# Performance work log

Measured on AMD Instinct MI355X. Metric: run time of the kernel, lower is better.

The kernel has to match this reference:

```python
import jax, jax.numpy as jnp
import numpy as np

N_SRC, N_DST, E = 100000, 50000, 1000000
IN_F, H, D = 256, 4, 32
NEG_SLOPE = 0.2


def setup_inputs() -> dict:
    key = jax.random.key(0)
    k = jax.random.split(key, 7)
    x = jax.random.normal(k[0], (N_SRC, IN_F), dtype=jnp.float32)
    # scale weights so exp() of attention logits stays well-conditioned
    fc_w = jax.random.normal(k[1], (H * D, IN_F), dtype=jnp.float32) * (1.0 / np.sqrt(IN_F))
    attn_l = jax.random.normal(k[2], (1, H, D), dtype=jnp.float32) * 0.1
    attn_r = jax.random.normal(k[3], (1, H, D), dtype=jnp.float32) * 0.1
    src_idx = jax.random.randint(k[4], (E,), 0, N_SRC, dtype=jnp.int32)
    dst_idx = jax.random.randint(k[5], (E,), 0, N_DST, dtype=jnp.int32)
    dst_node_ids = jax.random.randint(k[6], (N_DST,), 0, N_SRC, dtype=jnp.int32)
    return {"x": x, "fc_w": fc_w, "attn_l": attn_l, "attn_r": attn_r,
            "src_idx": src_idx, "dst_idx": dst_idx, "dst_node_ids": dst_node_ids}


def reference(x, fc_w, attn_l, attn_r, src_idx, dst_idx, dst_node_ids):
    # fc: [N_src, in] @ [in, H*D] -> [N_src, H, D]
    h = (x @ fc_w.T).reshape(-1, H, D)
    # per-node, per-head attention scalars
    el = jnp.einsum('nhd,ohd->nh', h, attn_l)            # [N_src, H]
    h_dst = h[dst_node_ids]                               # self_gather -> [N_dst, H, D]
    er = jnp.einsum('nhd,ohd->nh', h_dst, attn_r)        # [N_dst, H]
    # apply_edge: e = el[src] + er[dst], then leaky_relu + exp (edge softmax numerator)
    e = el[src_idx] + er[dst_idx]                         # [E, H]
    e = jnp.where(e >= 0, e, NEG_SLOPE * e)
    exp_e = jnp.exp(e)
    # apply_node: segment-sum denominators over destination nodes
    sum_exp = jax.ops.segment_sum(exp_e, dst_idx, num_segments=N_DST)  # [N_dst, H]
    att = exp_e / sum_exp[dst_idx]                        # [E, H]
    # attention_gather: weighted scatter-add of source features to dst nodes
    msg = att[:, :, None] * h[src_idx]                    # [E, H, D]
    out = jax.ops.segment_sum(msg, dst_idx, num_segments=N_DST)        # [N_dst, H, D]
    return out.reshape(N_DST, H * D)
```

## Files before the change

kernel.cpp:

```cpp
#include <hip/hip_runtime.h>
#include <hip/hip_bf16.h>

#define N_SRC_N  100000
#define N_DST_N  50000
#define NE       1000000
#define IN_F     256
#define NH       4
#define ND       32
#define HD       128
#define NEG_SLOPE 0.2f
#define L2E      1.44269504f

#define DPB      32
#define NB       1563
#define CAP      1024

typedef __attribute__((ext_vector_type(8))) short short8v;
typedef __attribute__((ext_vector_type(4))) short short4v;
typedef __attribute__((ext_vector_type(4))) float f32x4;

__device__ __forceinline__ short f2bf(float f) {
    __hip_bfloat16 h = __float2bfloat16(f);
    return *reinterpret_cast<short*>(&h);
}
__device__ __forceinline__ float bflo(unsigned u) { return __uint_as_float(u << 16); }
__device__ __forceinline__ float bfhi(unsigned u) { return __uint_as_float(u & 0xffff0000u); }

__global__ __launch_bounds__(256) void cvt_w(const float* __restrict__ w,
                                             short* __restrict__ wb)
{
    int i4 = blockIdx.x * 256 + threadIdx.x;
    if (i4 < (HD * IN_F) / 4) {
        f32x4 v = ((const f32x4*)w)[i4];
        short4v s;
        s[0] = f2bf(v[0]); s[1] = f2bf(v[1]); s[2] = f2bf(v[2]); s[3] = f2bf(v[3]);
        ((short4v*)wb)[i4] = s;
    }
}

__global__ __launch_bounds__(256) void gemm_fc_mfma(
    const float* __restrict__ x, const short* __restrict__ wb,
    const float* __restrict__ al, short* __restrict__ hb,
    float* __restrict__ el)
{
    __shared__ short wlds[HD * IN_F];

    const int tid = threadIdx.x;
    {
        int row = tid >> 1, half = tid & 1;
#pragma unroll
        for (int c = 0; c < 16; ++c) {
            int chunk = half * 16 + c;
            short8v v = *(const short8v*)(wb + row * IN_F + chunk * 8);
            int boff = (chunk * 16) ^ ((row & 7) << 4);
            *(short8v*)((char*)wlds + row * 512 + boff) = v;
        }
    }
    __syncthreads();

    const int w  = tid >> 6;
    const int l  = tid & 63;
    const int lr = l & 15;
    const int lk = l >> 4;

    float alv[8];
#pragma unroll
    for (int ct = 0; ct < 8; ++ct) alv[ct] = al[ct * 16 + lr];

    const int wave_id = blockIdx.x * 4 + w;
    for (int tile = wave_id; tile < N_SRC_N / 16; tile += 2048) {
        const int row0 = tile * 16;
        const float* xp = x + (size_t)(row0 + lr) * IN_F + lk * 8;

        f32x4 a[16];
#pragma unroll
        for (int kk = 0; kk < 8; ++kk) {
            a[2 * kk]     = *(const f32x4*)(xp + kk * 32);
            a[2 * kk + 1] = *(const f32x4*)(xp + kk * 32 + 4);
        }
        __builtin_amdgcn_sched_barrier(0);

        f32x4 acc[8];
#pragma unroll
        for (int ct = 0; ct < 8; ++ct) acc[ct] = (f32x4){0.f, 0.f, 0.f, 0.f};

#pragma unroll
        for (int kk = 0; kk < 8; ++kk) {
            f32x4 u0 = a[2 * kk], u1 = a[2 * kk + 1];
            short8v af;
            af[0] = f2bf(u0[0]); af[1] = f2bf(u0[1]);
            af[2] = f2bf(u0[2]); af[3] = f2bf(u0[3]);
            af[4] = f2bf(u1[0]); af[5] = f2bf(u1[1]);
            af[6] = f2bf(u1[2]); af[7] = f2bf(u1[3]);
            const int boff = (kk * 64 + lk * 16) ^ ((lr & 7) << 4);
#pragma unroll
            for (int ct = 0; ct < 8; ++ct) {
                short8v bf = *(const short8v*)((const char*)wlds
                                               + (ct * 16 + lr) * 512 + boff);
                acc[ct] = __builtin_amdgcn_mfma_f32_16x16x32_bf16(af, bf, acc[ct], 0, 0, 0);
            }
        }

#pragma unroll
        for (int r = 0; r < 4; ++r) {
            short* hp = hb + (size_t)(row0 + lk * 4 + r) * HD + lr;
#pragma unroll
            for (int ct = 0; ct < 8; ++ct) hp[ct * 16] = f2bf(acc[ct][r]);
        }

#pragma unroll
        for (int h = 0; h < 4; ++h) {
            float p[4];
#pragma unroll
            for (int r = 0; r < 4; ++r)
                p[r] = acc[2 * h][r] * alv[2 * h] + acc[2 * h + 1][r] * alv[2 * h + 1];
#pragma unroll
            for (int o = 1; o < 16; o <<= 1) {
#pragma unroll
                for (int r = 0; r < 4; ++r) p[r] += __shfl_xor(p[r], o, 64);
            }
            if (lr == 0) {
#pragma unroll
                for (int r = 0; r < 4; ++r)
                    el[(row0 + lk * 4 + r) * NH + h] = p[r];
            }
        }
    }
}

__global__ __launch_bounds__(256) void er_kernel(
    const short* __restrict__ hb, const float* __restrict__ ar,
    const int* __restrict__ dnid, float* __restrict__ er, int ndst)
{
    int i = blockIdx.x * 4 + (threadIdx.x >> 6);
    if (i >= ndst) return;
    int l = threadIdx.x & 63;
    int n = dnid[i];
    unsigned u = *(const unsigned*)(hb + (size_t)n * HD + 2 * l);
    float s = bflo(u) * ar[2 * l] + bfhi(u) * ar[2 * l + 1];
#pragma unroll
    for (int o = 1; o < 16; o <<= 1) s += __shfl_xor(s, o, 64);
    if ((l & 15) == 0) er[i * NH + (l >> 4)] = s;
}

__global__ __launch_bounds__(256) void bucket_hist(
    const int4* __restrict__ dst4, int* __restrict__ bcnt, int n4)
{
    __shared__ int lh[NB];
    for (int i = threadIdx.x; i < NB; i += 256) lh[i] = 0;
    __syncthreads();
#pragma unroll
    for (int q = 0; q < 4; ++q) {
        int e4 = blockIdx.x * 1024 + q * 256 + threadIdx.x;
        if (e4 < n4) {
            int4 v = dst4[e4];
            atomicAdd(&lh[v.x >> 5], 1); atomicAdd(&lh[v.y >> 5], 1);
            atomicAdd(&lh[v.z >> 5], 1); atomicAdd(&lh[v.w >> 5], 1);
        }
    }
    __syncthreads();
    for (int i = threadIdx.x; i < NB; i += 256) {
        int c = lh[i];
        if (c > 0) atomicAdd(&bcnt[i], c);
    }
}

__global__ __launch_bounds__(1024) void bucket_scan(
    const int* __restrict__ bcnt, int* __restrict__ boff, int* __restrict__ bcur, int n)
{
    int tid = threadIdx.x;
    int i0 = 2 * tid, i1 = 2 * tid + 1;
    int a = (i0 < n) ? bcnt[i0] : 0;
    int c = (i1 < n) ? bcnt[i1] : 0;
    int s = a + c, v = s;
#pragma unroll
    for (int o = 1; o < 64; o <<= 1) {
        int t = __shfl_up(v, o, 64);
        if ((tid & 63) >= o) v += t;
    }
    __shared__ int ws[16];
    if ((tid & 63) == 63) ws[tid >> 6] = v;
    __syncthreads();
    int add = 0;
    for (int q = 0; q < (tid >> 6); ++q) add += ws[q];
    int excl = v - s + add;
    if (i0 < n) { boff[i0] = excl;     bcur[i0] = excl; }
    if (i1 < n) { boff[i1] = excl + a; bcur[i1] = excl + a; }
}

__global__ __launch_bounds__(256) void partition(
    const int4* __restrict__ src4, const int4* __restrict__ dst4,
    int* __restrict__ bcur, int* __restrict__ ebuf, int n4)
{
    __shared__ int lh[NB];
    __shared__ int base[NB];
    for (int i = threadIdx.x; i < NB; i += 256) lh[i] = 0;
    __syncthreads();
    int4 sv[4], dv[4];
#pragma unroll
    for (int q = 0; q < 4; ++q) {
        int e4 = blockIdx.x * 1024 + q * 256 + threadIdx.x;
        if (e4 < n4) {
            sv[q] = src4[e4]; dv[q] = dst4[e4];
            atomicAdd(&lh[dv[q].x >> 5], 1); atomicAdd(&lh[dv[q].y >> 5], 1);
            atomicAdd(&lh[dv[q].z >> 5], 1); atomicAdd(&lh[dv[q].w >> 5], 1);
        } else {
            dv[q].x = -1;
        }
    }
    __syncthreads();
    for (int i = threadIdx.x; i < NB; i += 256) {
        int cnt = lh[i];
        base[i] = (cnt > 0) ? atomicAdd(&bcur[i], cnt) : 0;
        lh[i] = 0;
    }
    __syncthreads();
#pragma unroll
    for (int q = 0; q < 4; ++q) {
        if (dv[q].x < 0) continue;
        int ss[4] = {sv[q].x, sv[q].y, sv[q].z, sv[q].w};
        int dd[4] = {dv[q].x, dv[q].y, dv[q].z, dv[q].w};
#pragma unroll
        for (int j = 0; j < 4; ++j) {
            int b = dd[j] >> 5;
            int off = atomicAdd(&lh[b], 1);
            ebuf[base[b] + off] = ss[j] | ((dd[j] & 31) << 17);
        }
    }
}

__global__ __launch_bounds__(256) void gat_gather(
    const short* __restrict__ hb, const float* __restrict__ el,
    const float* __restrict__ er, const int* __restrict__ ebuf,
    const int* __restrict__ bcnt, const int* __restrict__ boff,
    float* __restrict__ out, int ndst)
{
    __shared__ int stage_[CAP];
    __shared__ int ssrc[CAP];
    __shared__ int lh[DPB];
    __shared__ int loff[DPB + 1];
    __shared__ int curs[DPB];

    const int b = blockIdx.x;
    const int tid = threadIdx.x;
    const int cnt = bcnt[b];
    const int gbase = boff[b];
    const int lcnt = (cnt < CAP) ? cnt : CAP;

    if (tid < DPB) lh[tid] = 0;
    __syncthreads();
    for (int i = tid; i < lcnt; i += 256) {
        int p = ebuf[gbase + i];
        stage_[i] = p;
        atomicAdd(&lh[(p >> 17) & 31], 1);
    }
    __syncthreads();
    if (tid < DPB) {
        int v = lh[tid];
#pragma unroll
        for (int o = 1; o < 32; o <<= 1) {
            int t = __shfl_up(v, o, 64);
            if (tid >= o) v += t;
        }
        loff[tid + 1] = v;
        if (tid == 0) loff[0] = 0;
    }
    __syncthreads();
    if (tid < DPB) curs[tid] = loff[tid];
    __syncthreads();
    for (int i = tid; i < lcnt; i += 256) {
        int p = stage_[i];
        int dl = (p >> 17) & 31;
        int pos = atomicAdd(&curs[dl], 1);
        ssrc[pos] = (p & 0x1FFFF) << 8;
    }
    __syncthreads();

    const int wv = tid >> 6;
    const int l  = tid & 63;
    const int head = l >> 4;
    const char* hbase = (const char*)hb + 4 * l;
    const char* ebase = (const char*)el + head * 4;

    for (int dl = wv; dl < DPB; dl += 4) {
        int d = b * DPB + dl;
        if (d >= ndst) continue;
        int j0 = loff[dl], j1 = loff[dl + 1];
        float erv = er[d * NH + head];

        float sumA = 0.f, sumB = 0.f;
        float acc0A = 0.f, acc1A = 0.f, acc0B = 0.f, acc1B = 0.f;
        int j = j0;
        for (; j + 8 <= j1; j += 8) {
            int off[8]; unsigned u[8]; float ev[8];
#pragma unroll
            for (int q = 0; q < 8; ++q) off[q] = ssrc[j + q];
#pragma unroll
            for (int q = 0; q < 8; ++q)
                u[q] = *(const unsigned*)(hbase + off[q]);
#pragma unroll
            for (int q = 0; q < 8; ++q)
                ev[q] = *(const float*)(ebase + (off[q] >> 4));
#pragma unroll
            for (int q = 0; q < 8; ++q) {
                float e = ev[q] + erv;
                e = fmaxf(e, NEG_SLOPE * e);
                float wq = __expf(e);
                if (q & 1) {
                    sumB += wq;
                    acc0B = fmaf(wq, bflo(u[q]), acc0B);
                    acc1B = fmaf(wq, bfhi(u[q]), acc1B);
                } else {
                    sumA += wq;
                    acc0A = fmaf(wq, bflo(u[q]), acc0A);
                    acc1A = fmaf(wq, bfhi(u[q]), acc1A);
                }
            }
        }
        for (; j < j1; ++j) {
            int off0 = ssrc[j];
            unsigned u0 = *(const unsigned*)(hbase + off0);
            float e0 = *(const float*)(ebase + (off0 >> 4)) + erv;
            e0 = fmaxf(e0, NEG_SLOPE * e0);
            float w0 = __expf(e0);
            sumA += w0;
            acc0A = fmaf(w0, bflo(u0), acc0A); acc1A = fmaf(w0, bfhi(u0), acc1A);
        }
        if (cnt > CAP) {
            for (int t = CAP; t < cnt; ++t) {
                int p = ebuf[gbase + t];
                if (((p >> 17) & 31) == dl) {
                    int off0 = (p & 0x1FFFF) << 8;
                    unsigned u0 = *(const unsigned*)(hbase + off0);
                    float e0 = *(const float*)(ebase + (off0 >> 4)) + erv;
                    e0 = fmaxf(e0, NEG_SLOPE * e0);
                    float w0 = __expf(e0);
                    sumA += w0;
                    acc0A = fmaf(w0, bflo(u0), acc0A); acc1A = fmaf(w0, bfhi(u0), acc1A);
                }
            }
        }
        float sum = sumA + sumB;
        bool any = (j1 > j0) || (cnt > CAP);
        float inv = any ? 1.f / sum : 0.f;
        float2 o2 = make_float2((acc0A + acc0B) * inv, (acc1A + acc1B) * inv);
        *(float2*)(out + (size_t)d * HD + 2 * l) = o2;
    }
}

extern "C" void kernel_launch(void* const* d_in, const int* in_sizes, int n_in,
                              void* d_out, int out_size, void* d_ws, size_t ws_size,
                              hipStream_t stream)
{
    const float* x   = (const float*)d_in[0];
    const float* fw  = (const float*)d_in[1];
    const float* al  = (const float*)d_in[2];
    const float* ar  = (const float*)d_in[3];
    const int*   src = (const int*)d_in[4];
    const int*   dst = (const int*)d_in[5];
    const int*   dnid= (const int*)d_in[6];
    float* out = (float*)d_out;

    char* ws = (char*)d_ws;
    size_t off = 0;
    auto alloc = [&](size_t bytes) -> void* {
        void* p = ws + off;
        off = (off + bytes + 255) & ~(size_t)255;
        return p;
    };
    short* hb   = (short*)alloc((size_t)N_SRC_N * HD * sizeof(short));
    short* wb   = (short*)alloc((size_t)HD * IN_F * sizeof(short));
    float* el   = (float*)alloc((size_t)N_SRC_N * NH * sizeof(float));
    float* er   = (float*)alloc((size_t)N_DST_N * NH * sizeof(float));
    int*   ebuf = (int*)alloc((size_t)NE * sizeof(int));
    int*   bcnt = (int*)alloc((size_t)NB * sizeof(int));
    int*   boff = (int*)alloc((size_t)NB * sizeof(int));
    int*   bcur = (int*)alloc((size_t)NB * sizeof(int));

    hipMemsetAsync(bcnt, 0, (size_t)NB * sizeof(int), stream);

    cvt_w<<<(HD * IN_F / 4 + 255) / 256, 256, 0, stream>>>(fw, wb);
    gemm_fc_mfma<<<512, 256, 0, stream>>>(x, wb, al, hb, el);
    er_kernel<<<(N_DST_N + 3) / 4, 256, 0, stream>>>(hb, ar, dnid, er, N_DST_N);
    bucket_hist<<<(NE / 4 + 1023) / 1024, 256, 0, stream>>>((const int4*)dst, bcnt, NE / 4);
    bucket_scan<<<1, 1024, 0, stream>>>(bcnt, boff, bcur, NB);
    partition<<<(NE / 4 + 1023) / 1024, 256, 0, stream>>>((const int4*)src, (const int4*)dst,
                                                          bcur, ebuf, NE / 4);
    gat_gather<<<NB, 256, 0, stream>>>(hb, el, er, ebuf, bcnt, boff, out, N_DST_N);
}
```

Baseline: 130.4 us.

## Fuse er computation into gather, widen GEMM blocks and partition chunks

Drops the separate er_kernel and computes each destination's er score inside gat_gather by loading the gathered node's bf16 features and reducing against attn_r with wave shuffles. This removes one launch and the er buffer round trip. The GEMM now runs 512-thread blocks with 8 waves sharing each LDS weight copy. The partition kernel handles twice as many edges per block, halving its grid and the number of global bucket-cursor atomics. The trade-offs are register pressure in partition (8 int4 pairs held per thread) and fewer waves in flight for that kernel.

```diff
diff --git a/kernel.cpp b/kernel.cpp
--- a/kernel.cpp
+++ b/kernel.cpp
@@ -9,7 +9,6 @@
 #define ND       32
 #define HD       128
 #define NEG_SLOPE 0.2f
-#define L2E      1.44269504f
 
 #define DPB      32
 #define NB       1563
@@ -38,7 +37,7 @@
     }
 }
 
-__global__ __launch_bounds__(256) void gemm_fc_mfma(
+__global__ __launch_bounds__(512, 4) void gemm_fc_mfma(
     const float* __restrict__ x, const short* __restrict__ wb,
     const float* __restrict__ al, short* __restrict__ hb,
     float* __restrict__ el)
@@ -47,10 +46,10 @@
 
     const int tid = threadIdx.x;
     {
-        int row = tid >> 1, half = tid & 1;
-#pragma unroll
-        for (int c = 0; c < 16; ++c) {
-            int chunk = half * 16 + c;
+        int row = tid >> 2, qt = tid & 3;
+#pragma unroll
+        for (int c = 0; c < 8; ++c) {
+            int chunk = qt * 8 + c;
             short8v v = *(const short8v*)(wb + row * IN_F + chunk * 8);
             int boff = (chunk * 16) ^ ((row & 7) << 4);
             *(short8v*)((char*)wlds + row * 512 + boff) = v;
@@ -67,8 +66,8 @@
 #pragma unroll
     for (int ct = 0; ct < 8; ++ct) alv[ct] = al[ct * 16 + lr];
 
-    const int wave_id = blockIdx.x * 4 + w;
-    for (int tile = wave_id; tile < N_SRC_N / 16; tile += 2048) {
+    const int wave_id = blockIdx.x * 8 + w;
+    for (int tile = wave_id; tile < N_SRC_N / 16; tile += 4096) {
         const int row0 = tile * 16;
         const float* xp = x + (size_t)(row0 + lr) * IN_F + lk * 8;
 
@@ -128,21 +127,6 @@
     }
 }
 
-__global__ __launch_bounds__(256) void er_kernel(
-    const short* __restrict__ hb, const float* __restrict__ ar,
-    const int* __restrict__ dnid, float* __restrict__ er, int ndst)
-{
-    int i = blockIdx.x * 4 + (threadIdx.x >> 6);
-    if (i >= ndst) return;
-    int l = threadIdx.x & 63;
-    int n = dnid[i];
-    unsigned u = *(const unsigned*)(hb + (size_t)n * HD + 2 * l);
-    float s = bflo(u) * ar[2 * l] + bfhi(u) * ar[2 * l + 1];
-#pragma unroll
-    for (int o = 1; o < 16; o <<= 1) s += __shfl_xor(s, o, 64);
-    if ((l & 15) == 0) er[i * NH + (l >> 4)] = s;
-}
-
 __global__ __launch_bounds__(256) void bucket_hist(
     const int4* __restrict__ dst4, int* __restrict__ bcnt, int n4)
 {
@@ -196,10 +180,10 @@
     __shared__ int base[NB];
     for (int i = threadIdx.x; i < NB; i += 256) lh[i] = 0;
     __syncthreads();
-    int4 sv[4], dv[4];
-#pragma unroll
-    for (int q = 0; q < 4; ++q) {
-        int e4 = blockIdx.x * 1024 + q * 256 + threadIdx.x;
+    int4 sv[8], dv[8];
+#pragma unroll
+    for (int q = 0; q < 8; ++q) {
+        int e4 = blockIdx.x * 2048 + q * 256 + threadIdx.x;
         if (e4 < n4) {
             sv[q] = src4[e4]; dv[q] = dst4[e4];
             atomicAdd(&lh[dv[q].x >> 5], 1); atomicAdd(&lh[dv[q].y >> 5], 1);
@@ -216,7 +200,7 @@
     }
     __syncthreads();
 #pragma unroll
-    for (int q = 0; q < 4; ++q) {
+    for (int q = 0; q < 8; ++q) {
         if (dv[q].x < 0) continue;
         int ss[4] = {sv[q].x, sv[q].y, sv[q].z, sv[q].w};
         int dd[4] = {dv[q].x, dv[q].y, dv[q].z, dv[q].w};
@@ -231,9 +215,9 @@
 
 __global__ __launch_bounds__(256) void gat_gather(
     const short* __restrict__ hb, const float* __restrict__ el,
-    const float* __restrict__ er, const int* __restrict__ ebuf,
-    const int* __restrict__ bcnt, const int* __restrict__ boff,
-    float* __restrict__ out, int ndst)
+    const float* __restrict__ ar, const int* __restrict__ dnid,
+    const int* __restrict__ ebuf, const int* __restrict__ bcnt,
+    const int* __restrict__ boff, float* __restrict__ out, int ndst)
 {
     __shared__ int stage_[CAP];
     __shared__ int ssrc[CAP];
@@ -281,12 +265,18 @@
     const int head = l >> 4;
     const char* hbase = (const char*)hb + 4 * l;
     const char* ebase = (const char*)el + head * 4;
+    const float ar0 = ar[2 * l], ar1 = ar[2 * l + 1];
 
     for (int dl = wv; dl < DPB; dl += 4) {
         int d = b * DPB + dl;
         if (d >= ndst) continue;
         int j0 = loff[dl], j1 = loff[dl + 1];
-        float erv = er[d * NH + head];
+
+        int nid = dnid[d];
+        unsigned ue = *(const unsigned*)(hbase + (size_t)nid * 256);
+        float erv = bflo(ue) * ar0 + bfhi(ue) * ar1;
+#pragma unroll
+        for (int o = 1; o < 16; o <<= 1) erv += __shfl_xor(erv, o, 64);
 
         float sumA = 0.f, sumB = 0.f;
         float acc0A = 0.f, acc1A = 0.f, acc0B = 0.f, acc1B = 0.f;
@@ -371,7 +361,6 @@
     short* hb   = (short*)alloc((size_t)N_SRC_N * HD * sizeof(short));
     short* wb   = (short*)alloc((size_t)HD * IN_F * sizeof(short));
     float* el   = (float*)alloc((size_t)N_SRC_N * NH * sizeof(float));
-    float* er   = (float*)alloc((size_t)N_DST_N * NH * sizeof(float));
     int*   ebuf = (int*)alloc((size_t)NE * sizeof(int));
     int*   bcnt = (int*)alloc((size_t)NB * sizeof(int));
     int*   boff = (int*)alloc((size_t)NB * sizeof(int));
@@ -380,11 +369,10 @@
     hipMemsetAsync(bcnt, 0, (size_t)NB * sizeof(int), stream);
 
     cvt_w<<<(HD * IN_F / 4 + 255) / 256, 256, 0, stream>>>(fw, wb);
-    gemm_fc_mfma<<<512, 256, 0, stream>>>(x, wb, al, hb, el);
-    er_kernel<<<(N_DST_N + 3) / 4, 256, 0, stream>>>(hb, ar, dnid, er, N_DST_N);
+    gemm_fc_mfma<<<512, 512, 0, stream>>>(x, wb, al, hb, el);
     bucket_hist<<<(NE / 4 + 1023) / 1024, 256, 0, stream>>>((const int4*)dst, bcnt, NE / 4);
     bucket_scan<<<1, 1024, 0, stream>>>(bcnt, boff, bcur, NB);
-    partition<<<(NE / 4 + 1023) / 1024, 256, 0, stream>>>((const int4*)src, (const int4*)dst,
+    partition<<<(NE / 4 + 2047) / 2048, 256, 0, stream>>>((const int4*)src, (const int4*)dst,
                                                           bcur, ebuf, NE / 4);
-    gat_gather<<<NB, 256, 0, stream>>>(hb, el, er, ebuf, bcnt, boff, out, N_DST_N);
-}
+    gat_gather<<<NB, 256, 0, stream>>>(hb, el, ar, dnid, ebuf, bcnt, boff, out, N_DST_N);
+}
```

New measurement: 125.9 us. 3.5% less time.
